# Performance work log

Measured on AMD Instinct MI355X. Metric: run time of the kernel, lower is better.

Reference implementation:

```python
import jax, jax.numpy as jnp
import numpy as np


def setup_inputs() -> dict:
    key = jax.random.key(0)
    k1, k2 = jax.random.split(key)
    B, T, S, D = 8, 1024, 1024, 2048
    support_sets = jax.random.normal(k1, (B, S, D), dtype=jnp.float32)
    X_hats = jax.random.normal(k2, (B, T, D), dtype=jnp.float32)
    return {"support_sets": support_sets, "X_hats": X_hats}


def reference(support_sets, X_hats):
    # Pairwise cosine similarity: out[b, t, s] = cos(X_hats[b, t], support_sets[b, s])
    # Matches torch.nn.functional.cosine_similarity with eps=1e-10:
    #   dot / max(||x|| * ||y||, eps)
    eps = 1e-10
    x_norm = jnp.linalg.norm(X_hats, axis=-1)          # [B, T]
    s_norm = jnp.linalg.norm(support_sets, axis=-1)    # [B, S]
    dots = jnp.einsum('btd,bsd->bts', X_hats, support_sets)  # [B, T, S]
    denom = jnp.maximum(x_norm[:, :, None] * s_norm[:, None, :], eps)
    return dots / denom
```

## Files before the change

### kernel.cpp

```cpp
#include <hip/hip_runtime.h>
#include <hip/hip_bf16.h>

typedef __attribute__((ext_vector_type(4))) float        f32x4;
typedef __attribute__((ext_vector_type(8))) short        s16x8;
typedef __attribute__((ext_vector_type(4))) unsigned int u32x4;
typedef __attribute__((ext_vector_type(2))) unsigned int u32x2;

#define Bb 8
#define Tt 1024
#define Ss 1024
#define Dd 2048
#define BM 128
#define BN 128
#define BK 64

__device__ __forceinline__ unsigned pack2_bf16(float f0, float f1) {
  unsigned u0 = __builtin_bit_cast(unsigned, f0) + 0x8000u;
  unsigned u1 = __builtin_bit_cast(unsigned, f1) + 0x8000u;
  return (u0 >> 16) | (u1 & 0xffff0000u);
}

__device__ __forceinline__ void gld_lds16(const void* g, void* l) {
  __builtin_amdgcn_global_load_lds(
      (__attribute__((address_space(1))) void*)(void*)(g),
      (__attribute__((address_space(3))) void*)l, 16, 0, 0);
}

__global__ __launch_bounds__(256, 8)
void convert_kernel(const float* __restrict__ sup, const float* __restrict__ xh,
                    unsigned* __restrict__ abf, unsigned* __restrict__ bbf,
                    float* __restrict__ invA, float* __restrict__ invB)
{
  __shared__ float red[4];
  const int bid = blockIdx.x;
  const int row = bid & 8191;
  const float* src; unsigned* dst; float* inv;
  if (bid < 8192) { src = xh;  dst = abf; inv = invA; }
  else            { src = sup; dst = bbf; inv = invB; }

  const int t = threadIdx.x;
  const f32x4* s = (const f32x4*)(src + (size_t)row * Dd);
  const f32x4 a = s[t];
  const f32x4 b = s[256 + t];

  float sq = fmaf(a[0], a[0], fmaf(a[1], a[1], fmaf(a[2], a[2], a[3] * a[3])));
  sq = fmaf(b[0], b[0], fmaf(b[1], b[1], fmaf(b[2], b[2], fmaf(b[3], b[3], sq))));

  u32x2* d = (u32x2*)(dst + (size_t)row * (Dd / 2));
  d[t]       = (u32x2){pack2_bf16(a[0], a[1]), pack2_bf16(a[2], a[3])};
  d[256 + t] = (u32x2){pack2_bf16(b[0], b[1]), pack2_bf16(b[2], b[3])};

  #pragma unroll
  for (int m = 32; m; m >>= 1) sq += __shfl_xor(sq, m, 64);
  const int wave = t >> 6, lane = t & 63;
  if (lane == 0) red[wave] = sq;
  __syncthreads();
  if (t == 0) inv[row] = 1.0f / sqrtf(red[0] + red[1] + red[2] + red[3]);
}

__global__ __launch_bounds__(256, 2)
void gemm_kernel(const short* __restrict__ abf, const short* __restrict__ bbf,
                 const float* __restrict__ invA, const float* __restrict__ invB,
                 float* __restrict__ out)
{
  __shared__ short As[2][BM * BK];
  __shared__ short Bs[2][BN * BK];

  const int bid0 = blockIdx.x;
  const int bid  = ((bid0 & 7) << 6) | (bid0 >> 3);
  const int b    = bid >> 6;
  const int tile = bid & 63;
  const int tm   = tile >> 3;
  const int tn   = tile & 7;

  const int t = threadIdx.x, wave = t >> 6, lane = t & 63;

  const int srow = lane >> 3;
  const int cph  = lane & 7;
  const int r0   = wave * 32;

  const size_t aRow = (size_t)(b * Tt + tm * BM);
  const size_t bRow = (size_t)(b * Ss + tn * BN);
  const short *gA0, *gA1, *gA2, *gA3, *gB0, *gB1, *gB2, *gB3;
  {
    int r;
    r = r0 + 0 * 8 + srow; gA0 = abf + (aRow + r) * Dd + (cph ^ (r & 7)) * 8;
                           gB0 = bbf + (bRow + r) * Dd + (cph ^ (r & 7)) * 8;
    r = r0 + 1 * 8 + srow; gA1 = abf + (aRow + r) * Dd + (cph ^ (r & 7)) * 8;
                           gB1 = bbf + (bRow + r) * Dd + (cph ^ (r & 7)) * 8;
    r = r0 + 2 * 8 + srow; gA2 = abf + (aRow + r) * Dd + (cph ^ (r & 7)) * 8;
                           gB2 = bbf + (bRow + r) * Dd + (cph ^ (r & 7)) * 8;
    r = r0 + 3 * 8 + srow; gA3 = abf + (aRow + r) * Dd + (cph ^ (r & 7)) * 8;
                           gB3 = bbf + (bRow + r) * Dd + (cph ^ (r & 7)) * 8;
  }

  const int wm = (wave >> 1) << 6;
  const int wn = (wave & 1) << 6;
  const int lm = lane & 15;
  const int kq = lane >> 4;

  f32x4 acc[4][4];
  #pragma unroll
  for (int i = 0; i < 4; ++i)
    #pragma unroll
    for (int j = 0; j < 4; ++j)
      acc[i][j] = (f32x4)0.0f;

#define STAGE(bi) do {                                                   \
    gld_lds16(gA0, As[bi] + (r0 + 0)  * BK);                             \
    gld_lds16(gA1, As[bi] + (r0 + 8)  * BK);                             \
    gld_lds16(gA2, As[bi] + (r0 + 16) * BK);                             \
    gld_lds16(gA3, As[bi] + (r0 + 24) * BK);                             \
    gld_lds16(gB0, Bs[bi] + (r0 + 0)  * BK);                             \
    gld_lds16(gB1, Bs[bi] + (r0 + 8)  * BK);                             \
    gld_lds16(gB2, Bs[bi] + (r0 + 16) * BK);                             \
    gld_lds16(gB3, Bs[bi] + (r0 + 24) * BK);                             \
    gA0 += BK; gA1 += BK; gA2 += BK; gA3 += BK;                          \
    gB0 += BK; gB1 += BK; gB2 += BK; gB3 += BK;                          \
  } while (0)

#define COMPUTE(bi) do {                                                 \
    _Pragma("unroll")                                                    \
    for (int ks = 0; ks < 2; ++ks) {                                     \
      const int pchunk = ((ks * 4 + kq) ^ (lm & 7)) * 8;                 \
      s16x8 af[4], bfr[4];                                               \
      _Pragma("unroll")                                                  \
      for (int i = 0; i < 4; ++i) {                                      \
        af[i]  = *(const s16x8*)(As[bi] + (wm + i * 16 + lm) * BK + pchunk); \
        bfr[i] = *(const s16x8*)(Bs[bi] + (wn + i * 16 + lm) * BK + pchunk); \
      }                                                                  \
      _Pragma("unroll")                                                  \
      for (int mi = 0; mi < 4; ++mi)                                     \
        _Pragma("unroll")                                                \
        for (int ni = 0; ni < 4; ++ni)                                   \
          acc[mi][ni] = __builtin_amdgcn_mfma_f32_16x16x32_bf16(af[mi], bfr[ni], acc[mi][ni], 0, 0, 0); \
    }                                                                    \
  } while (0)

#define WAIT_BAR(n) do {                                                 \
    asm volatile("s_waitcnt vmcnt(" #n ")" ::: "memory");                \
    __builtin_amdgcn_s_barrier();                                        \
    __builtin_amdgcn_sched_barrier(0);                                   \
  } while (0)

  STAGE(0);
  STAGE(1);

  for (int i = 0; i < 15; ++i) {
    WAIT_BAR(8);
    COMPUTE(0);
    __builtin_amdgcn_sched_barrier(0);
    __builtin_amdgcn_s_barrier();
    STAGE(0);
    WAIT_BAR(8);
    COMPUTE(1);
    __builtin_amdgcn_sched_barrier(0);
    __builtin_amdgcn_s_barrier();
    STAGE(1);
  }

  WAIT_BAR(8);
  COMPUTE(0);
  WAIT_BAR(0);
  COMPUTE(1);
#undef STAGE
#undef COMPUTE
#undef WAIT_BAR

  const float* iA = invA + b * Tt + tm * BM;
  const float* iB = invB + b * Ss + tn * BN;
  float* outb = out + (size_t)(b * Tt + tm * BM) * Ss + tn * BN;
  const int m0 = wm + kq * 4;
  const int n0 = wn + lm;
  #pragma unroll
  for (int mi = 0; mi < 4; ++mi) {
    #pragma unroll
    for (int r = 0; r < 4; ++r) {
      const int mrow = m0 + mi * 16 + r;
      const float ia = iA[mrow];
      float* orow = outb + (size_t)mrow * Ss;
      #pragma unroll
      for (int ni = 0; ni < 4; ++ni) {
        const int ncol = n0 + ni * 16;
        orow[ncol] = acc[mi][ni][r] * (ia * iB[ncol]);
      }
    }
  }
}

#define LDKF 40
#define BKF 32
__global__ __launch_bounds__(256, 2)
void paircos_kernel(const float* __restrict__ sup, const float* __restrict__ xh,
                    float* __restrict__ out)
{
  __shared__ short As[BM * LDKF];
  __shared__ short Bs[BN * LDKF];
  __shared__ float invA[BM];
  __shared__ float invB[BN];

  const int bid = blockIdx.x;
  const int b = bid >> 6, tile = bid & 63, tm = tile >> 3, tn = tile & 7;
  const float* Abase = xh  + (size_t)(b * Tt + tm * BM) * Dd;
  const float* Bbase = sup + (size_t)(b * Ss + tn * BN) * Dd;
  const int t = threadIdx.x, row = t >> 1, kh = t & 1;
  const f32x4* agp = (const f32x4*)(Abase + (size_t)row * Dd + kh * 16);
  const f32x4* bgp = (const f32x4*)(Bbase + (size_t)row * Dd + kh * 16);
  u32x4* awr = (u32x4*)(As + row * LDKF + kh * 16);
  u32x4* bwr = (u32x4*)(Bs + row * LDKF + kh * 16);
  const int wave = t >> 6, lane = t & 63;
  const int wm = (wave >> 1) << 6, wn = (wave & 1) << 6;
  const int lm = lane & 15, kq = lane >> 4;

  f32x4 acc[4][4];
  #pragma unroll
  for (int i = 0; i < 4; ++i)
    #pragma unroll
    for (int j = 0; j < 4; ++j) acc[i][j] = (f32x4)0.0f;
  float sqa = 0.0f, sqb = 0.0f;
  f32x4 areg[4], breg[4];
  #pragma unroll
  for (int i = 0; i < 4; ++i) { areg[i] = agp[i]; breg[i] = bgp[i]; }

  for (int k0 = 0; k0 < Dd; k0 += BKF) {
    unsigned pa[8], pb[8];
    #pragma unroll
    for (int i = 0; i < 4; ++i) {
      sqa = fmaf(areg[i][0], areg[i][0], sqa); sqa = fmaf(areg[i][1], areg[i][1], sqa);
      sqa = fmaf(areg[i][2], areg[i][2], sqa); sqa = fmaf(areg[i][3], areg[i][3], sqa);
      pa[i*2+0] = pack2_bf16(areg[i][0], areg[i][1]); pa[i*2+1] = pack2_bf16(areg[i][2], areg[i][3]);
      sqb = fmaf(breg[i][0], breg[i][0], sqb); sqb = fmaf(breg[i][1], breg[i][1], sqb);
      sqb = fmaf(breg[i][2], breg[i][2], sqb); sqb = fmaf(breg[i][3], breg[i][3], sqb);
      pb[i*2+0] = pack2_bf16(breg[i][0], breg[i][1]); pb[i*2+1] = pack2_bf16(breg[i][2], breg[i][3]);
    }
    __syncthreads();
    awr[0] = (u32x4){pa[0],pa[1],pa[2],pa[3]}; awr[1] = (u32x4){pa[4],pa[5],pa[6],pa[7]};
    bwr[0] = (u32x4){pb[0],pb[1],pb[2],pb[3]}; bwr[1] = (u32x4){pb[4],pb[5],pb[6],pb[7]};
    __syncthreads();
    if (k0 + BKF < Dd) {
      const int off = (k0 + BKF) >> 2;
      #pragma unroll
      for (int i = 0; i < 4; ++i) { areg[i] = agp[off + i]; breg[i] = bgp[off + i]; }
    }
    s16x8 af[4], bfr[4];
    #pragma unroll
    for (int i = 0; i < 4; ++i) {
      af[i]  = *(const s16x8*)(As + (wm + i*16 + lm) * LDKF + kq * 8);
      bfr[i] = *(const s16x8*)(Bs + (wn + i*16 + lm) * LDKF + kq * 8);
    }
    #pragma unroll
    for (int mi = 0; mi < 4; ++mi)
      #pragma unroll
      for (int ni = 0; ni < 4; ++ni)
        acc[mi][ni] = __builtin_amdgcn_mfma_f32_16x16x32_bf16(af[mi], bfr[ni], acc[mi][ni], 0, 0, 0);
  }
  __syncthreads();
  ((float*)As)[t] = sqa; ((float*)Bs)[t] = sqb;
  __syncthreads();
  if (t < 128) {
    invA[t] = 1.0f / sqrtf(((float*)As)[2*t] + ((float*)As)[2*t+1]);
    invB[t] = 1.0f / sqrtf(((float*)Bs)[2*t] + ((float*)Bs)[2*t+1]);
  }
  __syncthreads();
  float* outb = out + (size_t)(b * Tt + tm * BM) * Ss + tn * BN;
  const int m0 = wm + kq * 4, n0 = wn + lm;
  #pragma unroll
  for (int mi = 0; mi < 4; ++mi) {
    #pragma unroll
    for (int r = 0; r < 4; ++r) {
      const int mrow = m0 + mi * 16 + r;
      const float ia = invA[mrow];
      float* orow = outb + (size_t)mrow * Ss;
      #pragma unroll
      for (int ni = 0; ni < 4; ++ni) {
        const int ncol = n0 + ni * 16;
        orow[ncol] = acc[mi][ni][r] * (ia * invB[ncol]);
      }
    }
  }
}

extern "C" void kernel_launch(void* const* d_in, const int* in_sizes, int n_in,
                              void* d_out, int out_size, void* d_ws, size_t ws_size,
                              hipStream_t stream) {
  const float* sup = (const float*)d_in[0];
  const float* xh  = (const float*)d_in[1];
  float* out = (float*)d_out;

  const size_t nElem = (size_t)Bb * Tt * Dd;
  const size_t bfBytes = nElem * sizeof(short);
  const size_t NEED = 2 * bfBytes + 2 * (size_t)Bb * Tt * sizeof(float);

  if (ws_size >= NEED) {
    unsigned* abf = (unsigned*)d_ws;
    unsigned* bbf = (unsigned*)((char*)d_ws + bfBytes);
    float* invA = (float*)((char*)d_ws + 2 * bfBytes);
    float* invB = invA + (size_t)Bb * Tt;
    convert_kernel<<<dim3(16384), dim3(256), 0, stream>>>(sup, xh, abf, bbf, invA, invB);
    gemm_kernel<<<dim3(512), dim3(256), 0, stream>>>((const short*)abf, (const short*)bbf,
                                                     invA, invB, out);
  } else {
    paircos_kernel<<<dim3(512), dim3(256), 0, stream>>>(sup, xh, out);
  }
}
```

Measured before the change: 192.4 us.

## Restructure convert kernel into per-wave multi-row LDS double-buffered pipeline

The fp32-to-bf16 convert and norm kernel now has each wave handle four rows instead of one block per row. Rows are staged into LDS with asynchronous global_load_lds and double-buffered, with explicit vmcnt waits so the next row's loads overlap the current row's processing. The per-row norm reduction becomes a single-wave shuffle with no block barrier, and the grid shrinks from 16384 to 1024 blocks. In exchange, the kernel uses 64KB of LDS per block, which limits occupancy, and its correctness depends on hand-counted vmcnt values.

```diff
diff --git a/kernel.cpp b/kernel.cpp
--- a/kernel.cpp
+++ b/kernel.cpp
@@ -26,36 +26,59 @@
       (__attribute__((address_space(3))) void*)l, 16, 0, 0);
 }
 
-__global__ __launch_bounds__(256, 8)
+__global__ __launch_bounds__(256, 2)
 void convert_kernel(const float* __restrict__ sup, const float* __restrict__ xh,
                     unsigned* __restrict__ abf, unsigned* __restrict__ bbf,
                     float* __restrict__ invA, float* __restrict__ invB)
 {
-  __shared__ float red[4];
-  const int bid = blockIdx.x;
-  const int row = bid & 8191;
-  const float* src; unsigned* dst; float* inv;
-  if (bid < 8192) { src = xh;  dst = abf; inv = invA; }
-  else            { src = sup; dst = bbf; inv = invB; }
-
-  const int t = threadIdx.x;
-  const f32x4* s = (const f32x4*)(src + (size_t)row * Dd);
-  const f32x4 a = s[t];
-  const f32x4 b = s[256 + t];
-
-  float sq = fmaf(a[0], a[0], fmaf(a[1], a[1], fmaf(a[2], a[2], a[3] * a[3])));
-  sq = fmaf(b[0], b[0], fmaf(b[1], b[1], fmaf(b[2], b[2], fmaf(b[3], b[3], sq))));
-
-  u32x2* d = (u32x2*)(dst + (size_t)row * (Dd / 2));
-  d[t]       = (u32x2){pack2_bf16(a[0], a[1]), pack2_bf16(a[2], a[3])};
-  d[256 + t] = (u32x2){pack2_bf16(b[0], b[1]), pack2_bf16(b[2], b[3])};
-
-  #pragma unroll
-  for (int m = 32; m; m >>= 1) sq += __shfl_xor(sq, m, 64);
-  const int wave = t >> 6, lane = t & 63;
-  if (lane == 0) red[wave] = sq;
-  __syncthreads();
-  if (t == 0) inv[row] = 1.0f / sqrtf(red[0] + red[1] + red[2] + red[3]);
+  __shared__ float lds[2][4][2048];
+  const int t = threadIdx.x, wave = t >> 6, lane = t & 63;
+  const int wbase = (blockIdx.x * 4 + wave) * 4;
+
+  const float* src; unsigned* dst; float* inv; int row0;
+  if (wbase < 8192) { src = xh;  dst = abf; inv = invA; row0 = wbase; }
+  else              { src = sup; dst = bbf; inv = invB; row0 = wbase - 8192; }
+
+#define STAGE(slot, r) do {                                              \
+    const float* gp = src + (size_t)(row0 + (r)) * Dd + lane * 4;        \
+    float* lp = &lds[slot][wave][0];                                     \
+    _Pragma("unroll")                                                    \
+    for (int i = 0; i < 8; ++i)                                          \
+      gld_lds16(gp + i * 256, lp + i * 256);                             \
+  } while (0)
+
+#define PROCESS(slot, r) do {                                            \
+    const float* L = &lds[slot][wave][0];                                \
+    unsigned* drow = dst + (size_t)(row0 + (r)) * (Dd / 2);              \
+    float sq = 0.0f;                                                     \
+    _Pragma("unroll")                                                    \
+    for (int i = 0; i < 8; ++i) {                                        \
+      f32x4 v = *(const f32x4*)(L + i * 256 + lane * 4);                 \
+      sq = fmaf(v[0], v[0], fmaf(v[1], v[1], fmaf(v[2], v[2], fmaf(v[3], v[3], sq)))); \
+      *(u32x2*)(drow + i * 128 + lane * 2) =                             \
+          (u32x2){pack2_bf16(v[0], v[1]), pack2_bf16(v[2], v[3])};       \
+    }                                                                    \
+    _Pragma("unroll")                                                    \
+    for (int m = 32; m; m >>= 1) sq += __shfl_xor(sq, m, 64);            \
+    if (lane == 0) inv[row0 + (r)] = 1.0f / sqrtf(sq);                   \
+  } while (0)
+
+#define VWAIT(n) do {                                                    \
+    asm volatile("s_waitcnt vmcnt(" #n ")" ::: "memory");                \
+    __builtin_amdgcn_sched_barrier(0);                                   \
+  } while (0)
+
+  STAGE(0, 0);
+  STAGE(1, 1);
+  VWAIT(8);  PROCESS(0, 0);
+  STAGE(0, 2);
+  VWAIT(17); PROCESS(1, 1);
+  STAGE(1, 3);
+  VWAIT(17); PROCESS(0, 2);
+  VWAIT(9);  PROCESS(1, 3);
+#undef STAGE
+#undef PROCESS
+#undef VWAIT
 }
 
 __global__ __launch_bounds__(256, 2)
@@ -296,7 +319,7 @@
     unsigned* bbf = (unsigned*)((char*)d_ws + bfBytes);
     float* invA = (float*)((char*)d_ws + 2 * bfBytes);
     float* invB = invA + (size_t)Bb * Tt;
-    convert_kernel<<<dim3(16384), dim3(256), 0, stream>>>(sup, xh, abf, bbf, invA, invB);
+    convert_kernel<<<dim3(1024), dim3(256), 0, stream>>>(sup, xh, abf, bbf, invA, invB);
     gemm_kernel<<<dim3(512), dim3(256), 0, stream>>>((const short*)abf, (const short*)bbf,
                                                      invA, invB, out);
   } else {
```

Measured after the change: 196.3 us. 2.0% more time.
